# Kernel optimization log

Measured on AMD Instinct MI355X. Metric: run time of the kernel, lower is better.

Reference implementation:

```python
import jax, jax.numpy as jnp
import numpy as np

SIMILARITY_THRESHOLD = 0.8
TEMPERATURE = 0.5
EPS = 1e-12  # matches F.normalize eps


def _l2_normalize(x):
    n = jnp.linalg.norm(x, axis=1, keepdims=True)
    return x / jnp.maximum(n, EPS)


def setup_inputs() -> dict:
    key = jax.random.key(0)
    k1, k2 = jax.random.split(key)
    latent_features = jax.random.normal(k1, (8192, 128), dtype=jnp.float32)
    abr_features = jax.random.normal(k2, (8192, 6), dtype=jnp.float32)
    return {"latent_features": latent_features, "abr_features": abr_features}


def reference(latent_features, abr_features):
    B = latent_features.shape[0]
    eye = jnp.eye(B, dtype=bool)

    abr_n = _l2_normalize(abr_features)
    abr_sim = abr_n @ abr_n.T                      # [B, B]
    pos_mask = (abr_sim > SIMILARITY_THRESHOLD) & ~eye

    lat_n = _l2_normalize(latent_features)
    lat_sim = (lat_n @ lat_n.T) / TEMPERATURE       # [B, B]

    # Per anchor i: logsumexp over row excluding the diagonal entry.
    neg_inf = jnp.float32(-jnp.inf)
    row_lse = jax.nn.logsumexp(jnp.where(eye, neg_inf, lat_sim), axis=1)  # [B]

    # For each positive pair (i, j): CE([s_ij, row_i_excl_diag], label=0)
    #   = -s_ij + logsumexp(concat(s_ij, row_i)) = -s_ij + logaddexp(s_ij, row_lse[i])
    pair_loss = -lat_sim + jnp.logaddexp(lat_sim, row_lse[:, None])        # [B, B]

    num_pos = jnp.sum(pos_mask)
    denom = jnp.maximum(num_pos, 1).astype(lat_sim.dtype)
    phenotype_loss = jnp.where(
        num_pos > 0,
        jnp.sum(jnp.where(pos_mask, pair_loss, 0.0)) / denom,
        jnp.float32(0.0),
    )
    mean_abr_similarity = jnp.where(
        num_pos > 0,
        jnp.sum(jnp.where(pos_mask, abr_sim, 0.0)) / denom,
        jnp.float32(0.0),
    )
    positive_pair_ratio = num_pos.astype(jnp.float32) / (B * (B - 1))
    return (phenotype_loss, mean_abr_similarity, num_pos, positive_pair_ratio)
```

## Files before the change

kernel.cpp:

```cpp
#include <hip/hip_runtime.h>
#include <hip/hip_bf16.h>
#include <math.h>

#define SIM_THR 0.8f
#define LAT_SCALE 1.6986436f
#define LN2 0.6931471805599453f
#define TILES 8

typedef __attribute__((ext_vector_type(8))) short short8v;
typedef __attribute__((ext_vector_type(4))) float f32x4;
typedef __attribute__((ext_vector_type(4))) _Float16 half4v;

__device__ __forceinline__ void glds16(const void* g, void* l) {
    __builtin_amdgcn_global_load_lds(
        (const __attribute__((address_space(1))) void*)g,
        (__attribute__((address_space(3))) void*)l, 16, 0, 0);
}

__device__ __forceinline__ float fexp2(float x) {
#if __has_builtin(__builtin_amdgcn_exp2f)
    return __builtin_amdgcn_exp2f(x);
#else
    return exp2f(x);
#endif
}

__global__ __launch_bounds__(256) void k_norm_lat(const float* __restrict__ in,
                                                  __hip_bfloat16* __restrict__ out, int B) {
    int row = blockIdx.x * 4 + (threadIdx.x >> 6);
    int lane = threadIdx.x & 63;
    if (row >= B) return;
    float2 v = reinterpret_cast<const float2*>(in + (size_t)row * 128)[lane];
    float ss = v.x * v.x + v.y * v.y;
#pragma unroll
    for (int m = 1; m < 64; m <<= 1) ss += __shfl_xor(ss, m);
    float sc = LAT_SCALE / fmaxf(sqrtf(ss), 1e-12f);
    __hip_bfloat162 o;
    o.x = __float2bfloat16(v.x * sc);
    o.y = __float2bfloat16(v.y * sc);
    reinterpret_cast<__hip_bfloat162*>(out + (size_t)row * 128)[lane] = o;
}

__global__ __launch_bounds__(256) void k_norm_abr(const float* __restrict__ in,
                                                  _Float16* __restrict__ out, int B) {
    int row = blockIdx.x * 256 + threadIdx.x;
    if (row >= B) return;
    float v[6];
    float ss = 0.f;
#pragma unroll
    for (int d = 0; d < 6; ++d) { v[d] = in[(size_t)row * 6 + d]; ss += v[d] * v[d]; }
    float sc = 1.0f / fmaxf(sqrtf(ss), 1e-12f);
#pragma unroll
    for (int d = 0; d < 6; ++d) out[(size_t)row * 16 + d] = (_Float16)(v[d] * sc);
#pragma unroll
    for (int d = 6; d < 16; ++d) out[(size_t)row * 16 + d] = (_Float16)0.f;
}

__global__ __launch_bounds__(256, 3) void k_sweep(
    const __hip_bfloat16* __restrict__ lnbf,
    const _Float16* __restrict__ abrf,
    float2* __restrict__ slab, float2* __restrict__ wsum, int B)
{
    __shared__ __hip_bfloat16 Bs[64 * 128];

    int jc = blockIdx.x, bi = blockIdx.y;
    int i0 = bi * 128;
    int tid = threadIdx.x;
    int w = tid >> 6, l = tid & 63;
    int lr = l & 15, lg = l >> 4;

    short8v a[4][2];
#pragma unroll
    for (int kk = 0; kk < 4; ++kk)
#pragma unroll
        for (int m = 0; m < 2; ++m)
            a[kk][m] = *reinterpret_cast<const short8v*>(
                lnbf + (size_t)(i0 + w * 32 + m * 16 + lr) * 128 + (kk * 4 + lg) * 8);

    half4v aa[2];
#pragma unroll
    for (int m = 0; m < 2; ++m)
        aa[m] = *reinterpret_cast<const half4v*>(
            abrf + (size_t)(i0 + w * 32 + m * 16 + lr) * 16 + lg * 4);

    {
        int j0 = jc * TILES * 64;
#pragma unroll
        for (int ro = 0; ro < 4; ++ro) {
            int rbase = w * 16 + ro * 4;
            int row = rbase + (l >> 4);
            int sch = (l & 15) ^ (row & 7);
            glds16(lnbf + (size_t)(j0 + row) * 128 + sch * 8, Bs + rbase * 128);
        }
    }

    float esum_r[2][4] = {{0.f}}, cnt_r[2][4] = {{0.f}};
    float sumd = 0.f, sumsim = 0.f;

#pragma unroll 1
    for (int t = 0; t < TILES; ++t) {
        int jt = jc * TILES + t;
        int j0 = jt * 64;
        bool dtile = ((jt >> 1) == bi);
        int joff = (jt & 1) * 64;

        __syncthreads();

        half4v bb[4];
#pragma unroll
        for (int n = 0; n < 4; ++n)
            bb[n] = *reinterpret_cast<const half4v*>(
                abrf + (size_t)(j0 + n * 16 + lr) * 16 + lg * 4);

        f32x4 acc[2][4];
#pragma unroll
        for (int m = 0; m < 2; ++m)
#pragma unroll
            for (int n = 0; n < 4; ++n) acc[m][n] = (f32x4){0.f, 0.f, 0.f, 0.f};
#pragma unroll
        for (int kk = 0; kk < 4; ++kk) {
            short8v b[4];
#pragma unroll
            for (int n = 0; n < 4; ++n) {
                int jl = n * 16 + lr;
                int ch = (kk * 4 + lg) ^ (jl & 7);
                b[n] = *reinterpret_cast<const short8v*>(Bs + jl * 128 + ch * 8);
            }
#pragma unroll
            for (int m = 0; m < 2; ++m)
#pragma unroll
                for (int n = 0; n < 4; ++n)
                    acc[m][n] = __builtin_amdgcn_mfma_f32_16x16x32_bf16(a[kk][m], b[n], acc[m][n], 0, 0, 0);
        }
        __syncthreads();

        if (t + 1 < TILES) {
            int j0n = (jt + 1) * 64;
#pragma unroll
            for (int ro = 0; ro < 4; ++ro) {
                int rbase = w * 16 + ro * 4;
                int row = rbase + (l >> 4);
                int sch = (l & 15) ^ (row & 7);
                glds16(lnbf + (size_t)(j0n + row) * 128 + sch * 8, Bs + rbase * 128);
            }
        }

#pragma unroll
        for (int m = 0; m < 2; ++m) {
#pragma unroll
            for (int n = 0; n < 4; ++n) {
                f32x4 aacc = __builtin_amdgcn_mfma_f32_16x16x16f16(
                    aa[m], bb[n], (f32x4){0.f, 0.f, 0.f, 0.f}, 0, 0, 0);
#pragma unroll
                for (int r = 0; r < 4; ++r) {
                    float d = acc[m][n][r];
                    float sim = aacc[r];
                    float e = fexp2(d);
                    bool pred = sim > SIM_THR;
                    if (dtile) {
                        bool dg = (w * 32 + m * 16 + lg * 4 + r) == (joff + n * 16 + lr);
                        if (dg) { e = 0.f; pred = false; }
                    }
                    float p = pred ? 1.f : 0.f;
                    esum_r[m][r] += e;
                    cnt_r[m][r] += p;
                    sumsim = fmaf(p, sim, sumsim);
                    sumd = fmaf(p, d, sumd);
                }
            }
        }
    }

#pragma unroll
    for (int m = 0; m < 2; ++m)
#pragma unroll
        for (int r = 0; r < 4; ++r) {
            float a0 = esum_r[m][r], a1 = cnt_r[m][r];
#pragma unroll
            for (int d2 = 1; d2 < 16; d2 <<= 1) {
                a0 += __shfl_xor(a0, d2);
                a1 += __shfl_xor(a1, d2);
            }
            if (lr == 0) {
                int row_g = i0 + w * 32 + m * 16 + lg * 4 + r;
                slab[(size_t)jc * B + row_g] = make_float2(a0, a1);
            }
        }

#pragma unroll
    for (int d2 = 1; d2 < 64; d2 <<= 1) {
        sumd += __shfl_xor(sumd, d2);
        sumsim += __shfl_xor(sumsim, d2);
    }
    if (l == 0)
        wsum[(size_t)(bi * 16 + jc) * 4 + w] = make_float2(sumd, sumsim);
}

__global__ __launch_bounds__(256) void k_rows(const float2* __restrict__ slab,
                                              float* __restrict__ pC,
                                              float* __restrict__ pLN, int B) {
    __shared__ float sc[4], sl[4];
    int tid = threadIdx.x;
    int i = blockIdx.x * 256 + tid;
    float S = 0.f, c = 0.f;
#pragma unroll
    for (int k = 0; k < 16; ++k) {
        float2 v = slab[(size_t)k * B + i];
        S += v.x; c += v.y;
    }
    float ln = c * logf(S);
#pragma unroll
    for (int d = 1; d < 64; d <<= 1) {
        c += __shfl_xor(c, d); ln += __shfl_xor(ln, d);
    }
    int wave = tid >> 6, lane = tid & 63;
    if (lane == 0) { sc[wave] = c; sl[wave] = ln; }
    __syncthreads();
    if (tid == 0) {
        pC[blockIdx.x] = sc[0] + sc[1] + sc[2] + sc[3];
        pLN[blockIdx.x] = sl[0] + sl[1] + sl[2] + sl[3];
    }
}

__global__ __launch_bounds__(256) void k_final(const float* __restrict__ pC,
                                               const float* __restrict__ pLN,
                                               const float2* __restrict__ wsum,
                                               float* __restrict__ out,
                                               int nrb, int nw, float npairs) {
    __shared__ float s0[4], s1[4], s2[4], s3[4];
    int tid = threadIdx.x;
    float c = 0.f, ln = 0.f, sd = 0.f, sm = 0.f;
    for (int e = tid; e < nw; e += 256) {
        float2 v = wsum[e];
        sd += v.x; sm += v.y;
    }
    if (tid < nrb) { c = pC[tid]; ln = pLN[tid]; }
#pragma unroll
    for (int d = 1; d < 64; d <<= 1) {
        c += __shfl_xor(c, d); ln += __shfl_xor(ln, d);
        sd += __shfl_xor(sd, d); sm += __shfl_xor(sm, d);
    }
    int wave = tid >> 6, lane = tid & 63;
    if (lane == 0) { s0[wave] = c; s1[wave] = ln; s2[wave] = sd; s3[wave] = sm; }
    __syncthreads();
    if (tid == 0) {
        float ct = s0[0] + s0[1] + s0[2] + s0[3];
        float lt = s1[0] + s1[1] + s1[2] + s1[3];
        float st = s2[0] + s2[1] + s2[2] + s2[3];
        float mt = s3[0] + s3[1] + s3[2] + s3[3];
        out[0] = (ct > 0.f) ? (lt - LN2 * st) / ct : 0.f;
        out[1] = (ct > 0.f) ? mt / ct : 0.f;
        out[2] = ct;
        out[3] = ct / npairs;
    }
}

extern "C" void kernel_launch(void* const* d_in, const int* in_sizes, int n_in,
                              void* d_out, int out_size, void* d_ws, size_t ws_size,
                              hipStream_t stream) {
    const float* lat = (const float*)d_in[0];
    const float* abr = (const float*)d_in[1];
    float* out = (float*)d_out;
    int B = in_sizes[1] / 6;

    char* ws = (char*)d_ws;
    size_t off = 0;
    __hip_bfloat16* lnbf = (__hip_bfloat16*)(ws + off); off += (size_t)B * 128 * 2;
    _Float16* abrf = (_Float16*)(ws + off); off += (size_t)B * 16 * 2;
    float2* slab = (float2*)(ws + off); off += (size_t)16 * B * 8;
    int nblk = 16 * (B / 128);
    float2* wsum = (float2*)(ws + off); off += (size_t)nblk * 4 * 8;
    int nrb = B / 256;
    float* pC = (float*)(ws + off); off += (size_t)nrb * 4;
    float* pLN = (float*)(ws + off); off += (size_t)nrb * 4;

    k_norm_lat<<<B / 4, 256, 0, stream>>>(lat, lnbf, B);
    k_norm_abr<<<(B + 255) / 256, 256, 0, stream>>>(abr, abrf, B);
    k_sweep<<<dim3(16, B / 128), 256, 0, stream>>>(lnbf, abrf, slab, wsum, B);
    k_rows<<<nrb, 256, 0, stream>>>(slab, pC, pLN, B);
    k_final<<<1, 256, 0, stream>>>(pC, pLN, wsum, out, nrb, nblk * 4, (float)B * (float)(B - 1));
}
```

Before: 56.79 us.

## Exploit symmetry of similarity matrices: sweep upper triangle with row/column partials

The sweep now covers only the upper-triangular tile pairs (1056 blocks from a triangular index mapping) and accumulates both row and column partial exp-sums and positive counts. Column partials go through shared memory to a column slab, and k_rows gathers row and column contributions. The pair sums are doubled in the final kernel. The B tile is double-buffered so the next tile loads before compute, and the two normalization kernels are merged into one launch. This roughly halves the MFMA and exp work, at the cost of extra shuffles, shared-memory column accumulation and irregular per-row reads in k_rows.

```diff
diff --git a/kernel.cpp b/kernel.cpp
--- a/kernel.cpp
+++ b/kernel.cpp
@@ -5,7 +5,6 @@
 #define SIM_THR 0.8f
 #define LAT_SCALE 1.6986436f
 #define LN2 0.6931471805599453f
-#define TILES 8
 
 typedef __attribute__((ext_vector_type(8))) short short8v;
 typedef __attribute__((ext_vector_type(4))) float f32x4;
@@ -25,50 +24,66 @@
 #endif
 }
 
-__global__ __launch_bounds__(256) void k_norm_lat(const float* __restrict__ in,
-                                                  __hip_bfloat16* __restrict__ out, int B) {
-    int row = blockIdx.x * 4 + (threadIdx.x >> 6);
-    int lane = threadIdx.x & 63;
-    if (row >= B) return;
-    float2 v = reinterpret_cast<const float2*>(in + (size_t)row * 128)[lane];
-    float ss = v.x * v.x + v.y * v.y;
-#pragma unroll
-    for (int m = 1; m < 64; m <<= 1) ss += __shfl_xor(ss, m);
-    float sc = LAT_SCALE / fmaxf(sqrtf(ss), 1e-12f);
-    __hip_bfloat162 o;
-    o.x = __float2bfloat16(v.x * sc);
-    o.y = __float2bfloat16(v.y * sc);
-    reinterpret_cast<__hip_bfloat162*>(out + (size_t)row * 128)[lane] = o;
-}
-
-__global__ __launch_bounds__(256) void k_norm_abr(const float* __restrict__ in,
-                                                  _Float16* __restrict__ out, int B) {
-    int row = blockIdx.x * 256 + threadIdx.x;
-    if (row >= B) return;
-    float v[6];
-    float ss = 0.f;
-#pragma unroll
-    for (int d = 0; d < 6; ++d) { v[d] = in[(size_t)row * 6 + d]; ss += v[d] * v[d]; }
-    float sc = 1.0f / fmaxf(sqrtf(ss), 1e-12f);
-#pragma unroll
-    for (int d = 0; d < 6; ++d) out[(size_t)row * 16 + d] = (_Float16)(v[d] * sc);
-#pragma unroll
-    for (int d = 6; d < 16; ++d) out[(size_t)row * 16 + d] = (_Float16)0.f;
+__global__ __launch_bounds__(256) void k_norm(const float* __restrict__ lat,
+                                              const float* __restrict__ abr,
+                                              __hip_bfloat16* __restrict__ lout,
+                                              _Float16* __restrict__ aout, int B) {
+    int nb_lat = B / 4;
+    if ((int)blockIdx.x < nb_lat) {
+        int row = blockIdx.x * 4 + (threadIdx.x >> 6);
+        int lane = threadIdx.x & 63;
+        float2 v = reinterpret_cast<const float2*>(lat + (size_t)row * 128)[lane];
+        float ss = v.x * v.x + v.y * v.y;
+#pragma unroll
+        for (int m = 1; m < 64; m <<= 1) ss += __shfl_xor(ss, m);
+        float sc = LAT_SCALE / fmaxf(sqrtf(ss), 1e-12f);
+        __hip_bfloat162 o;
+        o.x = __float2bfloat16(v.x * sc);
+        o.y = __float2bfloat16(v.y * sc);
+        reinterpret_cast<__hip_bfloat162*>(lout + (size_t)row * 128)[lane] = o;
+    } else {
+        int row = (blockIdx.x - nb_lat) * 256 + threadIdx.x;
+        if (row >= B) return;
+        float v[6];
+        float ss = 0.f;
+#pragma unroll
+        for (int d = 0; d < 6; ++d) { v[d] = abr[(size_t)row * 6 + d]; ss += v[d] * v[d]; }
+        float sc = 1.0f / fmaxf(sqrtf(ss), 1e-12f);
+#pragma unroll
+        for (int d = 0; d < 6; ++d) aout[(size_t)row * 16 + d] = (_Float16)(v[d] * sc);
+#pragma unroll
+        for (int d = 6; d < 16; ++d) aout[(size_t)row * 16 + d] = (_Float16)0.f;
+    }
 }
 
 __global__ __launch_bounds__(256, 3) void k_sweep(
     const __hip_bfloat16* __restrict__ lnbf,
     const _Float16* __restrict__ abrf,
-    float2* __restrict__ slab, float2* __restrict__ wsum, int B)
+    float2* __restrict__ rowslab,
+    float2* __restrict__ colslab,
+    float2* __restrict__ wsum, int B)
 {
-    __shared__ __hip_bfloat16 Bs[64 * 128];
-
-    int jc = blockIdx.x, bi = blockIdx.y;
+    __shared__ __hip_bfloat16 Bs[2][64 * 128];
+    __shared__ float2 colaccw[4 * 256];
+
+    int blk = blockIdx.x;
+    int q = (int)((65.0 - sqrt(4225.0 - 4.0 * (double)blk)) * 0.5);
+    while (q * (65 - q) > blk) --q;
+    while ((q + 1) * (64 - q) <= blk) ++q;
+    int rr = blk - q * (65 - q);
+    int cc = 32 - q;
+    int bi = 2 * q + (rr >= cc ? 1 : 0);
+    int jc = q + (rr >= cc ? rr - cc : rr);
     int i0 = bi * 128;
+    int t0 = (jc == q && (bi & 1)) ? 2 : 0;
+
     int tid = threadIdx.x;
     int w = tid >> 6, l = tid & 63;
     int lr = l & 15, lg = l >> 4;
 
+#pragma unroll
+    for (int k = 0; k < 4; ++k) colaccw[k * 256 + tid] = make_float2(0.f, 0.f);
+
     short8v a[4][2];
 #pragma unroll
     for (int kk = 0; kk < 4; ++kk)
@@ -83,34 +98,37 @@
         aa[m] = *reinterpret_cast<const half4v*>(
             abrf + (size_t)(i0 + w * 32 + m * 16 + lr) * 16 + lg * 4);
 
-    {
-        int j0 = jc * TILES * 64;
+    auto stage = [&](int jt, int buf) {
+        int j0 = jt * 64;
 #pragma unroll
         for (int ro = 0; ro < 4; ++ro) {
             int rbase = w * 16 + ro * 4;
             int row = rbase + (l >> 4);
             int sch = (l & 15) ^ (row & 7);
-            glds16(lnbf + (size_t)(j0 + row) * 128 + sch * 8, Bs + rbase * 128);
-        }
-    }
+            glds16(lnbf + (size_t)(j0 + row) * 128 + sch * 8, &Bs[buf][rbase * 128]);
+        }
+    };
+
+    stage(jc * 4 + t0, 0);
 
     float esum_r[2][4] = {{0.f}}, cnt_r[2][4] = {{0.f}};
     float sumd = 0.f, sumsim = 0.f;
 
 #pragma unroll 1
-    for (int t = 0; t < TILES; ++t) {
-        int jt = jc * TILES + t;
-        int j0 = jt * 64;
-        bool dtile = ((jt >> 1) == bi);
-        int joff = (jt & 1) * 64;
+    for (int t = t0; t < 4; ++t) {
+        int jt = jc * 4 + t;
+        int cur = (t - t0) & 1;
+        bool gated = ((jt >> 1) == bi);
 
         __syncthreads();
+
+        if (t < 3) stage(jt + 1, cur ^ 1);
 
         half4v bb[4];
 #pragma unroll
         for (int n = 0; n < 4; ++n)
             bb[n] = *reinterpret_cast<const half4v*>(
-                abrf + (size_t)(j0 + n * 16 + lr) * 16 + lg * 4);
+                abrf + (size_t)(jt * 64 + n * 16 + lr) * 16 + lg * 4);
 
         f32x4 acc[2][4];
 #pragma unroll
@@ -124,7 +142,7 @@
             for (int n = 0; n < 4; ++n) {
                 int jl = n * 16 + lr;
                 int ch = (kk * 4 + lg) ^ (jl & 7);
-                b[n] = *reinterpret_cast<const short8v*>(Bs + jl * 128 + ch * 8);
+                b[n] = *reinterpret_cast<const short8v*>(&Bs[cur][jl * 128 + ch * 8]);
             }
 #pragma unroll
             for (int m = 0; m < 2; ++m)
@@ -132,19 +150,8 @@
                 for (int n = 0; n < 4; ++n)
                     acc[m][n] = __builtin_amdgcn_mfma_f32_16x16x32_bf16(a[kk][m], b[n], acc[m][n], 0, 0, 0);
         }
-        __syncthreads();
-
-        if (t + 1 < TILES) {
-            int j0n = (jt + 1) * 64;
-#pragma unroll
-            for (int ro = 0; ro < 4; ++ro) {
-                int rbase = w * 16 + ro * 4;
-                int row = rbase + (l >> 4);
-                int sch = (l & 15) ^ (row & 7);
-                glds16(lnbf + (size_t)(j0n + row) * 128 + sch * 8, Bs + rbase * 128);
-            }
-        }
-
+
+        float colb_e[4] = {0.f, 0.f, 0.f, 0.f}, colb_c[4] = {0.f, 0.f, 0.f, 0.f};
 #pragma unroll
         for (int m = 0; m < 2; ++m) {
 #pragma unroll
@@ -157,16 +164,30 @@
                     float sim = aacc[r];
                     float e = fexp2(d);
                     bool pred = sim > SIM_THR;
-                    if (dtile) {
-                        bool dg = (w * 32 + m * 16 + lg * 4 + r) == (joff + n * 16 + lr);
-                        if (dg) { e = 0.f; pred = false; }
+                    if (gated) {
+                        bool keep = (jt * 64 + n * 16 + lr) > (i0 + w * 32 + m * 16 + lg * 4 + r);
+                        if (!keep) { e = 0.f; pred = false; }
                     }
                     float p = pred ? 1.f : 0.f;
                     esum_r[m][r] += e;
                     cnt_r[m][r] += p;
                     sumsim = fmaf(p, sim, sumsim);
                     sumd = fmaf(p, d, sumd);
+                    colb_e[n] += e;
+                    colb_c[n] += p;
                 }
+            }
+        }
+#pragma unroll
+        for (int n = 0; n < 4; ++n) {
+            float ce = colb_e[n], cp = colb_c[n];
+            ce += __shfl_xor(ce, 16); ce += __shfl_xor(ce, 32);
+            cp += __shfl_xor(cp, 16); cp += __shfl_xor(cp, 32);
+            if (lg == 0) {
+                int idx = w * 256 + t * 64 + n * 16 + lr;
+                float2 v = colaccw[idx];
+                v.x += ce; v.y += cp;
+                colaccw[idx] = v;
             }
         }
     }
@@ -183,7 +204,7 @@
             }
             if (lr == 0) {
                 int row_g = i0 + w * 32 + m * 16 + lg * 4 + r;
-                slab[(size_t)jc * B + row_g] = make_float2(a0, a1);
+                rowslab[(size_t)jc * B + row_g] = make_float2(a0, a1);
             }
         }
 
@@ -192,23 +213,35 @@
         sumd += __shfl_xor(sumd, d2);
         sumsim += __shfl_xor(sumsim, d2);
     }
-    if (l == 0)
-        wsum[(size_t)(bi * 16 + jc) * 4 + w] = make_float2(sumd, sumsim);
-}
-
-__global__ __launch_bounds__(256) void k_rows(const float2* __restrict__ slab,
+    if (l == 0) wsum[(size_t)blk * 4 + w] = make_float2(sumd, sumsim);
+
+    __syncthreads();
+    {
+        float2 v0 = colaccw[tid], v1 = colaccw[256 + tid];
+        float2 v2 = colaccw[512 + tid], v3 = colaccw[768 + tid];
+        colslab[(size_t)bi * B + jc * 256 + tid] =
+            make_float2(v0.x + v1.x + v2.x + v3.x, v0.y + v1.y + v2.y + v3.y);
+    }
+}
+
+__global__ __launch_bounds__(256) void k_rows(const float2* __restrict__ rowslab,
+                                              const float2* __restrict__ colslab,
                                               float* __restrict__ pC,
                                               float* __restrict__ pLN, int B) {
     __shared__ float sc[4], sl[4];
     int tid = threadIdx.x;
     int i = blockIdx.x * 256 + tid;
+    int bi = i >> 7;
     float S = 0.f, c = 0.f;
-#pragma unroll
-    for (int k = 0; k < 16; ++k) {
-        float2 v = slab[(size_t)k * B + i];
+    for (int jc = bi >> 1; jc < 32; ++jc) {
+        float2 v = rowslab[(size_t)jc * B + i];
         S += v.x; c += v.y;
     }
-    float ln = c * logf(S);
+    for (int b2 = 0; b2 < bi; ++b2) {
+        float2 v = colslab[(size_t)b2 * B + i];
+        S += v.x; c += v.y;
+    }
+    float ln = (c > 0.f) ? c * logf(S) : 0.f;
 #pragma unroll
     for (int d = 1; d < 64; d <<= 1) {
         c += __shfl_xor(c, d); ln += __shfl_xor(ln, d);
@@ -246,8 +279,8 @@
     if (tid == 0) {
         float ct = s0[0] + s0[1] + s0[2] + s0[3];
         float lt = s1[0] + s1[1] + s1[2] + s1[3];
-        float st = s2[0] + s2[1] + s2[2] + s2[3];
-        float mt = s3[0] + s3[1] + s3[2] + s3[3];
+        float st = 2.f * (s2[0] + s2[1] + s2[2] + s2[3]);
+        float mt = 2.f * (s3[0] + s3[1] + s3[2] + s3[3]);
         out[0] = (ct > 0.f) ? (lt - LN2 * st) / ct : 0.f;
         out[1] = (ct > 0.f) ? mt / ct : 0.f;
         out[2] = ct;
@@ -267,16 +300,16 @@
     size_t off = 0;
     __hip_bfloat16* lnbf = (__hip_bfloat16*)(ws + off); off += (size_t)B * 128 * 2;
     _Float16* abrf = (_Float16*)(ws + off); off += (size_t)B * 16 * 2;
-    float2* slab = (float2*)(ws + off); off += (size_t)16 * B * 8;
-    int nblk = 16 * (B / 128);
+    float2* rowslab = (float2*)(ws + off); off += (size_t)32 * B * 8;
+    float2* colslab = (float2*)(ws + off); off += (size_t)64 * B * 8;
+    int nblk = 1056;
     float2* wsum = (float2*)(ws + off); off += (size_t)nblk * 4 * 8;
     int nrb = B / 256;
     float* pC = (float*)(ws + off); off += (size_t)nrb * 4;
     float* pLN = (float*)(ws + off); off += (size_t)nrb * 4;
 
-    k_norm_lat<<<B / 4, 256, 0, stream>>>(lat, lnbf, B);
-    k_norm_abr<<<(B + 255) / 256, 256, 0, stream>>>(abr, abrf, B);
-    k_sweep<<<dim3(16, B / 128), 256, 0, stream>>>(lnbf, abrf, slab, wsum, B);
-    k_rows<<<nrb, 256, 0, stream>>>(slab, pC, pLN, B);
+    k_norm<<<B / 4 + B / 256, 256, 0, stream>>>(lat, abr, lnbf, abrf, B);
+    k_sweep<<<nblk, 256, 0, stream>>>(lnbf, abrf, rowslab, colslab, wsum, B);
+    k_rows<<<nrb, 256, 0, stream>>>(rowslab, colslab, pC, pLN, B);
     k_final<<<1, 256, 0, stream>>>(pC, pLN, wsum, out, nrb, nblk * 4, (float)B * (float)(B - 1));
 }
```

After: 106.6 us. +87.8%, slower.
